# Kernel optimization log

Measured on AMD Instinct MI355X. Metric: run time of the kernel, lower is better.

Reference implementation:

```python
import jax, jax.numpy as jnp
import numpy as np

N_CHANNELS = 256
N_NEIGHBOURS = 262144
DIM = 3


def setup_inputs() -> dict:
    key = jax.random.key(0)
    k1, k2, k3 = jax.random.split(key, 3)
    h = jax.random.normal(k1, (N_CHANNELS, N_NEIGHBOURS), dtype=jnp.float32)
    rel_poss = jax.random.normal(k2, (DIM, N_NEIGHBOURS), dtype=jnp.float32)
    W = jax.random.normal(k3, (N_CHANNELS, N_CHANNELS), dtype=jnp.float32)
    return {"h": h, "rel_poss": rel_poss, "W": W}


def reference(h, rel_poss, W):
    # dists: [N], unit directions u: [dim, N]
    dists = jnp.linalg.norm(rel_poss, axis=0)
    u = rel_poss / dists
    # radial basis e_rbf(x, n, c=2) = (2/2)**0.5 * sin(n*x)/x = sin(n*x)/x, n = 1..K
    n = jnp.arange(1, N_CHANNELS + 1, dtype=h.dtype)
    radial_emb = jnp.sin(n[:, None] * dists[None, :]) / dists[None, :]  # [K, N]
    # channel-mixed features
    hp = W @ h  # [K, N]
    # per-neighbour: radial * feature scalar times rank-2 outer product u u^T, summed over neighbours
    m = radial_emb * hp  # [K, N]
    A = jnp.einsum('ki,di,ei->kde', m, u, u)  # [K, dim, dim]
    return A
```

## Files before the change

kernel.cpp:

```cpp
#include <hip/hip_runtime.h>
#include <hip/hip_bf16.h>

#define NCH      256
#define NNB      262144
#define BN       64
#define NTILES   (NNB / BN)
#define NB       512
#define ITPB     (NTILES / NB)
#define NENT     (NCH * 6)
#define NTHREADS 512

typedef __bf16        bf16x8 __attribute__((ext_vector_type(8)));
typedef float         f32x4  __attribute__((ext_vector_type(4)));
typedef unsigned int  u32x4  __attribute__((ext_vector_type(4)));
typedef unsigned int  u32x2  __attribute__((ext_vector_type(2)));
typedef short         v4s    __attribute__((ext_vector_type(4)));

union FragU  { u32x4 u; bf16x8 b; };
union Frag2U { u32x2 u; v4s    s; };

__device__ __forceinline__ unsigned pk2(float lo, float hi) {
    union { __hip_bfloat162 h2; unsigned u; } cv;
    cv.h2 = __float22bfloat162_rn(make_float2(lo, hi));
    return cv.u;
}

__device__ __forceinline__ const float* uni_ptr(const float* p) {
    unsigned long long u = (unsigned long long)p;
    unsigned lo = __builtin_amdgcn_readfirstlane((unsigned)u);
    unsigned hi = __builtin_amdgcn_readfirstlane((unsigned)(u >> 32));
    return (const float*)(((unsigned long long)hi << 32) | lo);
}

#define LBAR() do {                                                  \
    asm volatile("s_waitcnt lgkmcnt(0)" ::: "memory");               \
    __builtin_amdgcn_sched_barrier(0);                               \
    __builtin_amdgcn_s_barrier();                                    \
    __builtin_amdgcn_sched_barrier(0);                               \
} while (0)

#define CBODY(CB)                                                                  \
{                                                                                  \
    const int colb = (CB) * 16;                                                    \
    Frag2U gf;                                                                     \
    gf.u = *(const u32x2*)(gTP +                                                   \
           (((unsigned)(il * 128 + (colb + q * 4) * 2)) ^                          \
            (((unsigned)(il & 7)) << 3)));                                         \
    f32x4 hp0 = {0.f, 0.f, 0.f, 0.f}, hp1 = {0.f, 0.f, 0.f, 0.f};                  \
    const unsigned rb = (unsigned)((colb + il) * 512);                             \
    _Pragma("unroll")                                                              \
    for (int jb = 0; jb < 8; ++jb) {                                               \
        FragU f0;                                                                  \
        f0.u = *(const u32x4*)((const char*)htP +                                  \
               ((rb + (unsigned)(jb * 64 + q * 16)) ^ sw));                        \
        hp0 = __builtin_amdgcn_mfma_f32_16x16x32_bf16(f0.b, wf[0][jb].b, hp0, 0, 0, 0); \
        hp1 = __builtin_amdgcn_mfma_f32_16x16x32_bf16(f0.b, wf[1][jb].b, hp1, 0, 0, 0); \
    }                                                                              \
    f32x4 d4 = *(const f32x4*)(dtP + colb + q * 4);                                \
    f32x4 i4 = *(const f32x4*)(dtP + 64 + colb + q * 4);                           \
    Frag2U a0, a1;                                                                 \
    {                                                                              \
        float m0 = __sinf(fk0 * d4[0]) * i4[0] * hp0[0];                           \
        float m1 = __sinf(fk0 * d4[1]) * i4[1] * hp0[1];                           \
        float m2 = __sinf(fk0 * d4[2]) * i4[2] * hp0[2];                           \
        float m3 = __sinf(fk0 * d4[3]) * i4[3] * hp0[3];                           \
        a0.u[0] = pk2(m0, m1); a0.u[1] = pk2(m2, m3);                              \
        float n0 = __sinf(fk1 * d4[0]) * i4[0] * hp1[0];                           \
        float n1 = __sinf(fk1 * d4[1]) * i4[1] * hp1[1];                           \
        float n2 = __sinf(fk1 * d4[2]) * i4[2] * hp1[2];                           \
        float n3 = __sinf(fk1 * d4[3]) * i4[3] * hp1[3];                           \
        a1.u[0] = pk2(n0, n1); a1.u[1] = pk2(n2, n3);                              \
    }                                                                              \
    acc0 = __builtin_amdgcn_mfma_f32_16x16x16bf16_1k(a0.s, gf.s, acc0, 0, 0, 0);   \
    acc1 = __builtin_amdgcn_mfma_f32_16x16x16bf16_1k(a1.s, gf.s, acc1, 0, 0, 0);   \
}

#define CHUNK8_ISSUE(Q)                                                            \
    if (hasNext) {                                                                 \
        _Pragma("unroll")                                                          \
        for (int j = 0; j < 8; ++j)                                                \
            hc[j] = hwb[(size_t)((Q) * 8 + j) * NNB + baseN + c];                  \
    }

#define CHUNK8_PACK(Q)                                                             \
    if (hasNext) {                                                                 \
        u32x4 w0;                                                                  \
        w0[0] = pk2(hc[0], hc[1]); w0[1] = pk2(hc[2], hc[3]);                      \
        w0[2] = pk2(hc[4], hc[5]); w0[3] = pk2(hc[6], hc[7]);                      \
        *(u32x4*)((char*)htN +                                                     \
            (((unsigned)(c * 512 + wave * 64 + (Q) * 16)) ^ swc)) = w0;            \
    }

__global__ __launch_bounds__(NTHREADS, 2) void create_As_k1(
        const float* __restrict__ h, const float* __restrict__ rp,
        const float* __restrict__ W, float* __restrict__ ws)
{
    __shared__ unsigned short htile[2][BN * NCH];
    __shared__ unsigned short gT[2][16 * BN];
    __shared__ __align__(16) float dtab[2][2][BN];

    const int t    = threadIdx.x;
    const int wave = t >> 6;
    const int il   = t & 15;
    const int q    = (t >> 4) & 3;
    const int c    = t & 63;
    const int k0   = wave * 32;
    const unsigned sw  = ((unsigned)(il & 7)) << 4;
    const unsigned swc = ((unsigned)(c & 7)) << 4;
    const float fk0 = (float)(k0 + il + 1);
    const float fk1 = fk0 + 16.0f;

    #pragma unroll
    for (int z = 0; z < 2; ++z) ((unsigned*)gT)[t + z * NTHREADS] = 0u;

    FragU wf[2][8];
    #pragma unroll
    for (int kt = 0; kt < 2; ++kt) {
        const float* wr = W + (size_t)(k0 + kt * 16 + il) * NCH + q * 8;
        #pragma unroll
        for (int jb = 0; jb < 8; ++jb) {
            f32x4 a = *(const f32x4*)(wr + jb * 32);
            f32x4 b = *(const f32x4*)(wr + jb * 32 + 4);
            wf[kt][jb].u[0] = pk2(a[0], a[1]);
            wf[kt][jb].u[1] = pk2(a[2], a[3]);
            wf[kt][jb].u[2] = pk2(b[0], b[1]);
            wf[kt][jb].u[3] = pk2(b[2], b[3]);
        }
    }

    f32x4 acc0 = {0.f, 0.f, 0.f, 0.f};
    f32x4 acc1 = {0.f, 0.f, 0.f, 0.f};

    const float* hwb = uni_ptr(h + (size_t)(wave * 32) * NNB);

    const int d0 = blockIdx.x;

    __syncthreads();

    {
        const unsigned base = (unsigned)(d0 * BN);
        #pragma unroll
        for (int qq = 0; qq < 4; ++qq) {
            float hv[8];
            #pragma unroll
            for (int j = 0; j < 8; ++j)
                hv[j] = hwb[(size_t)(qq * 8 + j) * NNB + base + c];
            u32x4 w0;
            w0[0] = pk2(hv[0], hv[1]); w0[1] = pk2(hv[2], hv[3]);
            w0[2] = pk2(hv[4], hv[5]); w0[3] = pk2(hv[6], hv[7]);
            *(u32x4*)((char*)htile[0] +
                (((unsigned)(c * 512 + wave * 64 + qq * 16)) ^ swc)) = w0;
        }
        if (t < 64) {
            const unsigned ii = base + (unsigned)c;
            float gx = rp[ii], gy = rp[(size_t)NNB + ii], gz = rp[2 * (size_t)NNB + ii];
            float dd = sqrtf(gx * gx + gy * gy + gz * gz);
            float iv = 1.0f / dd;
            dtab[0][0][c] = dd; dtab[0][1][c] = iv;
            float i2 = iv * iv;
            float gg[6] = { gx * gx * i2, gx * gy * i2, gx * gz * i2,
                            gy * gy * i2, gy * gz * i2, gz * gz * i2 };
            #pragma unroll
            for (int de = 0; de < 6; ++de) {
                unsigned off = ((unsigned)(de * 128 + c * 2)) ^ (((unsigned)de) << 3);
                *(unsigned short*)((char*)gT[0] + off) =
                    (unsigned short)(pk2(gg[de], 0.f) & 0xffffu);
            }
        }
    }
    LBAR();

    #pragma unroll 1
    for (int it = 0; it < ITPB; ++it) {
        const int P = it & 1;
        const unsigned short* htP = htile[P];
        unsigned short*       htN = htile[P ^ 1];
        const char*  gTP = (const char*)gT[P];
        const float* dtP = &dtab[P][0][0];
        const bool hasNext = (it + 1 < ITPB);
        const unsigned baseN = (unsigned)((d0 + (it + 1) * NB) * BN);

        float gx = 0.f, gy = 0.f, gz = 0.f;
        if (hasNext && t < 64) {
            const unsigned ii = baseN + (unsigned)c;
            gx = rp[ii]; gy = rp[(size_t)NNB + ii]; gz = rp[2 * (size_t)NNB + ii];
        }

        float hc[8];
        CHUNK8_ISSUE(0)
        __builtin_amdgcn_sched_barrier(0);
        CBODY(0)
        __builtin_amdgcn_sched_barrier(0);
        CHUNK8_PACK(0) CHUNK8_ISSUE(1)
        __builtin_amdgcn_sched_barrier(0);
        CBODY(1)
        __builtin_amdgcn_sched_barrier(0);
        CHUNK8_PACK(1) CHUNK8_ISSUE(2)
        __builtin_amdgcn_sched_barrier(0);
        CBODY(2)
        __builtin_amdgcn_sched_barrier(0);
        CHUNK8_PACK(2) CHUNK8_ISSUE(3)
        __builtin_amdgcn_sched_barrier(0);
        CBODY(3)
        __builtin_amdgcn_sched_barrier(0);
        CHUNK8_PACK(3)
        if (hasNext && t < 64) {
            float dd = sqrtf(gx * gx + gy * gy + gz * gz);
            float iv = 1.0f / dd;
            dtab[P ^ 1][0][c] = dd; dtab[P ^ 1][1][c] = iv;
            float i2 = iv * iv;
            float gg[6] = { gx * gx * i2, gx * gy * i2, gx * gz * i2,
                            gy * gy * i2, gy * gz * i2, gz * gz * i2 };
            #pragma unroll
            for (int de = 0; de < 6; ++de) {
                unsigned off = ((unsigned)(de * 128 + c * 2)) ^ (((unsigned)de) << 3);
                *(unsigned short*)((char*)gT[P ^ 1] + off) =
                    (unsigned short)(pk2(gg[de], 0.f) & 0xffffu);
            }
        }
        LBAR();
    }

    if (il < 6) {
        float* dst = ws + (size_t)blockIdx.x * NENT;
        #pragma unroll
        for (int r = 0; r < 4; ++r) {
            dst[(k0 + q * 4 + r) * 6 + il]      = acc0[r];
            dst[(k0 + 16 + q * 4 + r) * 6 + il] = acc1[r];
        }
    }
}

__global__ void create_As_k2(const float* __restrict__ ws, float* __restrict__ out)
{
    __shared__ float red[8][64];
    const int eb = blockIdx.x;
    const int w  = threadIdx.x >> 6;
    const int l  = threadIdx.x & 63;
    float s = 0.f;
    #pragma unroll 4
    for (int b = w; b < NB; b += 8)
        s += ws[(size_t)b * NENT + (unsigned)(eb * 64 + l)];
    red[w][l] = s;
    __syncthreads();
    if (w == 0) {
        float v = red[0][l] + red[1][l] + red[2][l] + red[3][l]
                + red[4][l] + red[5][l] + red[6][l] + red[7][l];
        const int e  = eb * 64 + l;
        const int k  = e / 6;
        const int m6 = e - k * 6;
        const int d  = (m6 < 3) ? 0 : ((m6 < 5) ? 1 : 2);
        const int e2 = (m6 < 3) ? m6 : ((m6 < 5) ? (m6 - 2) : 2);
        out[k * 9 + d * 3 + e2] = v;
        if (d != e2) out[k * 9 + e2 * 3 + d] = v;
    }
}

extern "C" void kernel_launch(void* const* d_in, const int* in_sizes, int n_in,
                              void* d_out, int out_size, void* d_ws, size_t ws_size,
                              hipStream_t stream)
{
    const float* h  = (const float*)d_in[0];
    const float* rp = (const float*)d_in[1];
    const float* W  = (const float*)d_in[2];
    float* out = (float*)d_out;
    float* ws  = (float*)d_ws;

    hipLaunchKernelGGL(create_As_k1, dim3(NB), dim3(NTHREADS), 0, stream, h, rp, W, ws);
    hipLaunchKernelGGL(create_As_k2, dim3(NENT / 64), dim3(512), 0, stream, ws, out);
}
```

Before: 83.42 us.

## Double neighbour tile to 128 with float2 h loads and one block per CU

Raises the per-iteration neighbour tile from 64 to 128 columns and halves the grid to 256 blocks, each with occupancy hint 1. Global h loads become float2 per lane across two adjacent columns, and the LDS staging layout and swizzle are adjusted to match. The goal is fewer barriers per neighbour processed, wider global loads, and a longer software pipeline. In exchange, LDS use doubles and occupancy drops, which can expose latency. Note that the htile/gT/dtab declarations still use BN, so their sizes grow.

Measured after the change: 91.12 us. 9.2% more time.

```diff
diff --git a/kernel.cpp b/kernel.cpp
--- a/kernel.cpp
+++ b/kernel.cpp
@@ -3,15 +3,16 @@
 
 #define NCH      256
 #define NNB      262144
-#define BN       64
-#define NTILES   (NNB / BN)
-#define NB       512
-#define ITPB     (NTILES / NB)
+#define BN       128
+#define NDT      (NNB / BN)
+#define NB       256
+#define DTPB     (NDT / NB)
 #define NENT     (NCH * 6)
 #define NTHREADS 512
 
 typedef __bf16        bf16x8 __attribute__((ext_vector_type(8)));
 typedef float         f32x4  __attribute__((ext_vector_type(4)));
+typedef float         f32x2  __attribute__((ext_vector_type(2)));
 typedef unsigned int  u32x4  __attribute__((ext_vector_type(4)));
 typedef unsigned int  u32x2  __attribute__((ext_vector_type(2)));
 typedef short         v4s    __attribute__((ext_vector_type(4)));
@@ -44,7 +45,7 @@
     const int colb = (CB) * 16;                                                    \
     Frag2U gf;                                                                     \
     gf.u = *(const u32x2*)(gTP +                                                   \
-           (((unsigned)(il * 128 + (colb + q * 4) * 2)) ^                          \
+           (((unsigned)(il * 256 + (colb + q * 4) * 2)) ^                          \
             (((unsigned)(il & 7)) << 3)));                                         \
     f32x4 hp0 = {0.f, 0.f, 0.f, 0.f}, hp1 = {0.f, 0.f, 0.f, 0.f};                  \
     const unsigned rb = (unsigned)((colb + il) * 512);                             \
@@ -57,7 +58,7 @@
         hp1 = __builtin_amdgcn_mfma_f32_16x16x32_bf16(f0.b, wf[1][jb].b, hp1, 0, 0, 0); \
     }                                                                              \
     f32x4 d4 = *(const f32x4*)(dtP + colb + q * 4);                                \
-    f32x4 i4 = *(const f32x4*)(dtP + 64 + colb + q * 4);                           \
+    f32x4 i4 = *(const f32x4*)(dtP + BN + colb + q * 4);                           \
     Frag2U a0, a1;                                                                 \
     {                                                                              \
         float m0 = __sinf(fk0 * d4[0]) * i4[0] * hp0[0];                           \
@@ -75,23 +76,41 @@
     acc1 = __builtin_amdgcn_mfma_f32_16x16x16bf16_1k(a1.s, gf.s, acc1, 0, 0, 0);   \
 }
 
-#define CHUNK8_ISSUE(Q)                                                            \
+#define CHUNK4_ISSUE(Q)                                                            \
     if (hasNext) {                                                                 \
         _Pragma("unroll")                                                          \
-        for (int j = 0; j < 8; ++j)                                                \
-            hc[j] = hwb[(size_t)((Q) * 8 + j) * NNB + baseN + c];                  \
-    }
-
-#define CHUNK8_PACK(Q)                                                             \
+        for (int j2 = 0; j2 < 4; ++j2)                                             \
+            hc[j2] = *(const f32x2*)(hwb + (size_t)((Q) * 4 + j2) * NNB            \
+                                         + baseN + sc0);                           \
+    }
+
+#define CHUNK4_PACK(Q)                                                             \
     if (hasNext) {                                                                 \
-        u32x4 w0;                                                                  \
-        w0[0] = pk2(hc[0], hc[1]); w0[1] = pk2(hc[2], hc[3]);                      \
-        w0[2] = pk2(hc[4], hc[5]); w0[3] = pk2(hc[6], hc[7]);                      \
-        *(u32x4*)((char*)htN +                                                     \
-            (((unsigned)(c * 512 + wave * 64 + (Q) * 16)) ^ swc)) = w0;            \
-    }
-
-__global__ __launch_bounds__(NTHREADS, 2) void create_As_k1(
+        u32x2 wx, wy;                                                              \
+        wx[0] = pk2(hc[0][0], hc[1][0]); wx[1] = pk2(hc[2][0], hc[3][0]);          \
+        wy[0] = pk2(hc[0][1], hc[1][1]); wy[1] = pk2(hc[2][1], hc[3][1]);          \
+        const unsigned jo = (unsigned)(wave * 64 + (Q) * 8);                       \
+        *(u32x2*)((char*)htN + (((unsigned)(sc0 * 512)       + jo) ^ swp)) = wx;   \
+        *(u32x2*)((char*)htN + (((unsigned)(sc0 * 512 + 512) + jo) ^ swp)) = wy;   \
+    }
+
+#define GEOM(B)                                                                    \
+    if (t < 128) {                                                                 \
+        float dd = sqrtf(gx * gx + gy * gy + gz * gz);                             \
+        float iv = 1.0f / dd;                                                      \
+        dtab[B][0][t] = dd; dtab[B][1][t] = iv;                                    \
+        float i2 = iv * iv;                                                        \
+        float gg[6] = { gx * gx * i2, gx * gy * i2, gx * gz * i2,                  \
+                        gy * gy * i2, gy * gz * i2, gz * gz * i2 };                \
+        _Pragma("unroll")                                                          \
+        for (int de = 0; de < 6; ++de) {                                           \
+            unsigned off = ((unsigned)(de * 256 + t * 2)) ^ (((unsigned)de) << 3); \
+            *(unsigned short*)((char*)gT[B] + off) =                               \
+                (unsigned short)(pk2(gg[de], 0.f) & 0xffffu);                      \
+        }                                                                          \
+    }
+
+__global__ __launch_bounds__(NTHREADS, 1) void create_As_k1(
         const float* __restrict__ h, const float* __restrict__ rp,
         const float* __restrict__ W, float* __restrict__ ws)
 {
@@ -105,13 +124,14 @@
     const int q    = (t >> 4) & 3;
     const int c    = t & 63;
     const int k0   = wave * 32;
-    const unsigned sw  = ((unsigned)(il & 7)) << 4;
-    const unsigned swc = ((unsigned)(c & 7)) << 4;
+    const int sc0  = 2 * c;
+    const unsigned sw  = ((unsigned)((il >> 1) & 7)) << 4;
+    const unsigned swp = ((unsigned)(c & 7)) << 4;
     const float fk0 = (float)(k0 + il + 1);
     const float fk1 = fk0 + 16.0f;
 
     #pragma unroll
-    for (int z = 0; z < 2; ++z) ((unsigned*)gT)[t + z * NTHREADS] = 0u;
+    for (int z = 0; z < 4; ++z) ((unsigned*)gT)[t + z * NTHREADS] = 0u;
 
     FragU wf[2][8];
     #pragma unroll
@@ -140,84 +160,77 @@
     {
         const unsigned base = (unsigned)(d0 * BN);
         #pragma unroll
-        for (int qq = 0; qq < 4; ++qq) {
-            float hv[8];
+        for (int qq = 0; qq < 8; ++qq) {
+            f32x2 hv[4];
             #pragma unroll
-            for (int j = 0; j < 8; ++j)
-                hv[j] = hwb[(size_t)(qq * 8 + j) * NNB + base + c];
-            u32x4 w0;
-            w0[0] = pk2(hv[0], hv[1]); w0[1] = pk2(hv[2], hv[3]);
-            w0[2] = pk2(hv[4], hv[5]); w0[3] = pk2(hv[6], hv[7]);
-            *(u32x4*)((char*)htile[0] +
-                (((unsigned)(c * 512 + wave * 64 + qq * 16)) ^ swc)) = w0;
-        }
-        if (t < 64) {
-            const unsigned ii = base + (unsigned)c;
+            for (int j2 = 0; j2 < 4; ++j2)
+                hv[j2] = *(const f32x2*)(hwb + (size_t)(qq * 4 + j2) * NNB + base + sc0);
+            u32x2 wx, wy;
+            wx[0] = pk2(hv[0][0], hv[1][0]); wx[1] = pk2(hv[2][0], hv[3][0]);
+            wy[0] = pk2(hv[0][1], hv[1][1]); wy[1] = pk2(hv[2][1], hv[3][1]);
+            const unsigned jo = (unsigned)(wave * 64 + qq * 8);
+            *(u32x2*)((char*)htile[0] + (((unsigned)(sc0 * 512)       + jo) ^ swp)) = wx;
+            *(u32x2*)((char*)htile[0] + (((unsigned)(sc0 * 512 + 512) + jo) ^ swp)) = wy;
+        }
+        if (t < 128) {
+            const unsigned ii = base + (unsigned)t;
             float gx = rp[ii], gy = rp[(size_t)NNB + ii], gz = rp[2 * (size_t)NNB + ii];
-            float dd = sqrtf(gx * gx + gy * gy + gz * gz);
-            float iv = 1.0f / dd;
-            dtab[0][0][c] = dd; dtab[0][1][c] = iv;
-            float i2 = iv * iv;
-            float gg[6] = { gx * gx * i2, gx * gy * i2, gx * gz * i2,
-                            gy * gy * i2, gy * gz * i2, gz * gz * i2 };
-            #pragma unroll
-            for (int de = 0; de < 6; ++de) {
-                unsigned off = ((unsigned)(de * 128 + c * 2)) ^ (((unsigned)de) << 3);
-                *(unsigned short*)((char*)gT[0] + off) =
-                    (unsigned short)(pk2(gg[de], 0.f) & 0xffffu);
-            }
+            GEOM(0)
         }
     }
     LBAR();
 
     #pragma unroll 1
-    for (int it = 0; it < ITPB; ++it) {
+    for (int it = 0; it < DTPB; ++it) {
         const int P = it & 1;
         const unsigned short* htP = htile[P];
         unsigned short*       htN = htile[P ^ 1];
         const char*  gTP = (const char*)gT[P];
         const float* dtP = &dtab[P][0][0];
-        const bool hasNext = (it + 1 < ITPB);
+        const bool hasNext = (it + 1 < DTPB);
         const unsigned baseN = (unsigned)((d0 + (it + 1) * NB) * BN);
 
         float gx = 0.f, gy = 0.f, gz = 0.f;
-        if (hasNext && t < 64) {
-            const unsigned ii = baseN + (unsigned)c;
+        if (hasNext && t < 128) {
+            const unsigned ii = baseN + (unsigned)t;
             gx = rp[ii]; gy = rp[(size_t)NNB + ii]; gz = rp[2 * (size_t)NNB + ii];
         }
 
-        float hc[8];
-        CHUNK8_ISSUE(0)
+        f32x2 hc[4];
+        CHUNK4_ISSUE(0)
         __builtin_amdgcn_sched_barrier(0);
         CBODY(0)
         __builtin_amdgcn_sched_barrier(0);
-        CHUNK8_PACK(0) CHUNK8_ISSUE(1)
+        CHUNK4_PACK(0) CHUNK4_ISSUE(1)
         __builtin_amdgcn_sched_barrier(0);
         CBODY(1)
         __builtin_amdgcn_sched_barrier(0);
-        CHUNK8_PACK(1) CHUNK8_ISSUE(2)
+        CHUNK4_PACK(1) CHUNK4_ISSUE(2)
         __builtin_amdgcn_sched_barrier(0);
         CBODY(2)
         __builtin_amdgcn_sched_barrier(0);
-        CHUNK8_PACK(2) CHUNK8_ISSUE(3)
+        CHUNK4_PACK(2) CHUNK4_ISSUE(3)
         __builtin_amdgcn_sched_barrier(0);
         CBODY(3)
         __builtin_amdgcn_sched_barrier(0);
-        CHUNK8_PACK(3)
-        if (hasNext && t < 64) {
-            float dd = sqrtf(gx * gx + gy * gy + gz * gz);
-            float iv = 1.0f / dd;
-            dtab[P ^ 1][0][c] = dd; dtab[P ^ 1][1][c] = iv;
-            float i2 = iv * iv;
-            float gg[6] = { gx * gx * i2, gx * gy * i2, gx * gz * i2,
-                            gy * gy * i2, gy * gz * i2, gz * gz * i2 };
-            #pragma unroll
-            for (int de = 0; de < 6; ++de) {
-                unsigned off = ((unsigned)(de * 128 + c * 2)) ^ (((unsigned)de) << 3);
-                *(unsigned short*)((char*)gT[P ^ 1] + off) =
-                    (unsigned short)(pk2(gg[de], 0.f) & 0xffffu);
-            }
-        }
+        CHUNK4_PACK(3) CHUNK4_ISSUE(4)
+        __builtin_amdgcn_sched_barrier(0);
+        CBODY(4)
+        __builtin_amdgcn_sched_barrier(0);
+        CHUNK4_PACK(4) CHUNK4_ISSUE(5)
+        __builtin_amdgcn_sched_barrier(0);
+        CBODY(5)
+        __builtin_amdgcn_sched_barrier(0);
+        CHUNK4_PACK(5) CHUNK4_ISSUE(6)
+        __builtin_amdgcn_sched_barrier(0);
+        CBODY(6)
+        __builtin_amdgcn_sched_barrier(0);
+        CHUNK4_PACK(6) CHUNK4_ISSUE(7)
+        __builtin_amdgcn_sched_barrier(0);
+        CBODY(7)
+        __builtin_amdgcn_sched_barrier(0);
+        CHUNK4_PACK(7)
+        if (hasNext) { GEOM(P ^ 1) }
         LBAR();
     }
 
```

## Halve block to 4 waves, each computing 64 output channels

Applied to the files above, without the earlier changes.

Block size drops from 512 to 256 threads, and each wave now owns 64 channels of W instead of 32. Each LDS A-fragment of h is therefore reused across four MFMA weight tiles rather than two. The h prefetch for the next tile is restructured into two 16-element register buffers that are issued two chunks ahead. This cuts LDS reads per MFMA and wave count, at the cost of doubling the W fragment registers and prefetch registers, which may lower occupancy or cause spills.

New measurement: 283.7 us. 240% more time.

```diff
diff --git a/kernel.cpp b/kernel.cpp
--- a/kernel.cpp
+++ b/kernel.cpp
@@ -8,7 +8,7 @@
 #define NB       512
 #define ITPB     (NTILES / NB)
 #define NENT     (NCH * 6)
-#define NTHREADS 512
+#define NTHREADS 256
 
 typedef __bf16        bf16x8 __attribute__((ext_vector_type(8)));
 typedef float         f32x4  __attribute__((ext_vector_type(4)));
@@ -46,7 +46,8 @@
     gf.u = *(const u32x2*)(gTP +                                                   \
            (((unsigned)(il * 128 + (colb + q * 4) * 2)) ^                          \
             (((unsigned)(il & 7)) << 3)));                                         \
-    f32x4 hp0 = {0.f, 0.f, 0.f, 0.f}, hp1 = {0.f, 0.f, 0.f, 0.f};                  \
+    f32x4 hp0 = {0.f,0.f,0.f,0.f}, hp1 = {0.f,0.f,0.f,0.f};                        \
+    f32x4 hp2 = {0.f,0.f,0.f,0.f}, hp3 = {0.f,0.f,0.f,0.f};                        \
     const unsigned rb = (unsigned)((colb + il) * 512);                             \
     _Pragma("unroll")                                                              \
     for (int jb = 0; jb < 8; ++jb) {                                               \
@@ -55,40 +56,57 @@
                ((rb + (unsigned)(jb * 64 + q * 16)) ^ sw));                        \
         hp0 = __builtin_amdgcn_mfma_f32_16x16x32_bf16(f0.b, wf[0][jb].b, hp0, 0, 0, 0); \
         hp1 = __builtin_amdgcn_mfma_f32_16x16x32_bf16(f0.b, wf[1][jb].b, hp1, 0, 0, 0); \
+        hp2 = __builtin_amdgcn_mfma_f32_16x16x32_bf16(f0.b, wf[2][jb].b, hp2, 0, 0, 0); \
+        hp3 = __builtin_amdgcn_mfma_f32_16x16x32_bf16(f0.b, wf[3][jb].b, hp3, 0, 0, 0); \
     }                                                                              \
     f32x4 d4 = *(const f32x4*)(dtP + colb + q * 4);                                \
     f32x4 i4 = *(const f32x4*)(dtP + 64 + colb + q * 4);                           \
-    Frag2U a0, a1;                                                                 \
     {                                                                              \
-        float m0 = __sinf(fk0 * d4[0]) * i4[0] * hp0[0];                           \
-        float m1 = __sinf(fk0 * d4[1]) * i4[1] * hp0[1];                           \
-        float m2 = __sinf(fk0 * d4[2]) * i4[2] * hp0[2];                           \
-        float m3 = __sinf(fk0 * d4[3]) * i4[3] * hp0[3];                           \
-        a0.u[0] = pk2(m0, m1); a0.u[1] = pk2(m2, m3);                              \
-        float n0 = __sinf(fk1 * d4[0]) * i4[0] * hp1[0];                           \
-        float n1 = __sinf(fk1 * d4[1]) * i4[1] * hp1[1];                           \
-        float n2 = __sinf(fk1 * d4[2]) * i4[2] * hp1[2];                           \
-        float n3 = __sinf(fk1 * d4[3]) * i4[3] * hp1[3];                           \
-        a1.u[0] = pk2(n0, n1); a1.u[1] = pk2(n2, n3);                              \
+        Frag2U a;                                                                  \
+        float m0 = __sinf(fkb * d4[0]) * i4[0] * hp0[0];                           \
+        float m1 = __sinf(fkb * d4[1]) * i4[1] * hp0[1];                           \
+        float m2 = __sinf(fkb * d4[2]) * i4[2] * hp0[2];                           \
+        float m3 = __sinf(fkb * d4[3]) * i4[3] * hp0[3];                           \
+        a.u[0] = pk2(m0, m1); a.u[1] = pk2(m2, m3);                                \
+        acc0 = __builtin_amdgcn_mfma_f32_16x16x16bf16_1k(a.s, gf.s, acc0, 0, 0, 0);\
+        m0 = __sinf((fkb + 16.f) * d4[0]) * i4[0] * hp1[0];                        \
+        m1 = __sinf((fkb + 16.f) * d4[1]) * i4[1] * hp1[1];                        \
+        m2 = __sinf((fkb + 16.f) * d4[2]) * i4[2] * hp1[2];                        \
+        m3 = __sinf((fkb + 16.f) * d4[3]) * i4[3] * hp1[3];                        \
+        a.u[0] = pk2(m0, m1); a.u[1] = pk2(m2, m3);                                \
+        acc1 = __builtin_amdgcn_mfma_f32_16x16x16bf16_1k(a.s, gf.s, acc1, 0, 0, 0);\
+        m0 = __sinf((fkb + 32.f) * d4[0]) * i4[0] * hp2[0];                        \
+        m1 = __sinf((fkb + 32.f) * d4[1]) * i4[1] * hp2[1];                        \
+        m2 = __sinf((fkb + 32.f) * d4[2]) * i4[2] * hp2[2];                        \
+        m3 = __sinf((fkb + 32.f) * d4[3]) * i4[3] * hp2[3];                        \
+        a.u[0] = pk2(m0, m1); a.u[1] = pk2(m2, m3);                                \
+        acc2 = __builtin_amdgcn_mfma_f32_16x16x16bf16_1k(a.s, gf.s, acc2, 0, 0, 0);\
+        m0 = __sinf((fkb + 48.f) * d4[0]) * i4[0] * hp3[0];                        \
+        m1 = __sinf((fkb + 48.f) * d4[1]) * i4[1] * hp3[1];                        \
+        m2 = __sinf((fkb + 48.f) * d4[2]) * i4[2] * hp3[2];                        \
+        m3 = __sinf((fkb + 48.f) * d4[3]) * i4[3] * hp3[3];                        \
+        a.u[0] = pk2(m0, m1); a.u[1] = pk2(m2, m3);                                \
+        acc3 = __builtin_amdgcn_mfma_f32_16x16x16bf16_1k(a.s, gf.s, acc3, 0, 0, 0);\
     }                                                                              \
-    acc0 = __builtin_amdgcn_mfma_f32_16x16x16bf16_1k(a0.s, gf.s, acc0, 0, 0, 0);   \
-    acc1 = __builtin_amdgcn_mfma_f32_16x16x16bf16_1k(a1.s, gf.s, acc1, 0, 0, 0);   \
-}
-
-#define CHUNK8_ISSUE(Q)                                                            \
+}
+
+#define CHUNK16_ISSUE(DST, Q)                                                      \
     if (hasNext) {                                                                 \
         _Pragma("unroll")                                                          \
-        for (int j = 0; j < 8; ++j)                                                \
-            hc[j] = hwb[(size_t)((Q) * 8 + j) * NNB + baseN + c];                  \
-    }
-
-#define CHUNK8_PACK(Q)                                                             \
+        for (int j = 0; j < 16; ++j)                                               \
+            DST[j] = hwb[(size_t)((Q) * 16 + j) * NNB + baseN + c];                \
+    }
+
+#define CHUNK16_PACK(SRC, Q)                                                       \
     if (hasNext) {                                                                 \
-        u32x4 w0;                                                                  \
-        w0[0] = pk2(hc[0], hc[1]); w0[1] = pk2(hc[2], hc[3]);                      \
-        w0[2] = pk2(hc[4], hc[5]); w0[3] = pk2(hc[6], hc[7]);                      \
-        *(u32x4*)((char*)htN +                                                     \
-            (((unsigned)(c * 512 + wave * 64 + (Q) * 16)) ^ swc)) = w0;            \
+        u32x4 w0, w1;                                                              \
+        w0[0] = pk2(SRC[0],  SRC[1]);  w0[1] = pk2(SRC[2],  SRC[3]);               \
+        w0[2] = pk2(SRC[4],  SRC[5]);  w0[3] = pk2(SRC[6],  SRC[7]);               \
+        w1[0] = pk2(SRC[8],  SRC[9]);  w1[1] = pk2(SRC[10], SRC[11]);              \
+        w1[2] = pk2(SRC[12], SRC[13]); w1[3] = pk2(SRC[14], SRC[15]);              \
+        const unsigned boff = (unsigned)(c * 512 + wave * 128 + (Q) * 32);         \
+        *(u32x4*)((char*)htN + ((boff)      ^ swc)) = w0;                          \
+        *(u32x4*)((char*)htN + ((boff + 16) ^ swc)) = w1;                          \
     }
 
 __global__ __launch_bounds__(NTHREADS, 2) void create_As_k1(
@@ -104,18 +122,17 @@
     const int il   = t & 15;
     const int q    = (t >> 4) & 3;
     const int c    = t & 63;
-    const int k0   = wave * 32;
+    const int k0   = wave * 64;
     const unsigned sw  = ((unsigned)(il & 7)) << 4;
     const unsigned swc = ((unsigned)(c & 7)) << 4;
-    const float fk0 = (float)(k0 + il + 1);
-    const float fk1 = fk0 + 16.0f;
+    const float fkb = (float)(k0 + il + 1);
 
     #pragma unroll
-    for (int z = 0; z < 2; ++z) ((unsigned*)gT)[t + z * NTHREADS] = 0u;
-
-    FragU wf[2][8];
+    for (int z = 0; z < 4; ++z) ((unsigned*)gT)[t + z * NTHREADS] = 0u;
+
+    FragU wf[4][8];
     #pragma unroll
-    for (int kt = 0; kt < 2; ++kt) {
+    for (int kt = 0; kt < 4; ++kt) {
         const float* wr = W + (size_t)(k0 + kt * 16 + il) * NCH + q * 8;
         #pragma unroll
         for (int jb = 0; jb < 8; ++jb) {
@@ -128,10 +145,12 @@
         }
     }
 
-    f32x4 acc0 = {0.f, 0.f, 0.f, 0.f};
-    f32x4 acc1 = {0.f, 0.f, 0.f, 0.f};
-
-    const float* hwb = uni_ptr(h + (size_t)(wave * 32) * NNB);
+    f32x4 acc0 = {0.f,0.f,0.f,0.f};
+    f32x4 acc1 = {0.f,0.f,0.f,0.f};
+    f32x4 acc2 = {0.f,0.f,0.f,0.f};
+    f32x4 acc3 = {0.f,0.f,0.f,0.f};
+
+    const float* hwb = uni_ptr(h + (size_t)(wave * 64) * NNB);
 
     const int d0 = blockIdx.x;
 
@@ -141,15 +160,18 @@
         const unsigned base = (unsigned)(d0 * BN);
         #pragma unroll
         for (int qq = 0; qq < 4; ++qq) {
-            float hv[8];
+            float hv[16];
             #pragma unroll
-            for (int j = 0; j < 8; ++j)
-                hv[j] = hwb[(size_t)(qq * 8 + j) * NNB + base + c];
-            u32x4 w0;
-            w0[0] = pk2(hv[0], hv[1]); w0[1] = pk2(hv[2], hv[3]);
-            w0[2] = pk2(hv[4], hv[5]); w0[3] = pk2(hv[6], hv[7]);
-            *(u32x4*)((char*)htile[0] +
-                (((unsigned)(c * 512 + wave * 64 + qq * 16)) ^ swc)) = w0;
+            for (int j = 0; j < 16; ++j)
+                hv[j] = hwb[(size_t)(qq * 16 + j) * NNB + base + c];
+            u32x4 w0, w1;
+            w0[0] = pk2(hv[0],  hv[1]);  w0[1] = pk2(hv[2],  hv[3]);
+            w0[2] = pk2(hv[4],  hv[5]);  w0[3] = pk2(hv[6],  hv[7]);
+            w1[0] = pk2(hv[8],  hv[9]);  w1[1] = pk2(hv[10], hv[11]);
+            w1[2] = pk2(hv[12], hv[13]); w1[3] = pk2(hv[14], hv[15]);
+            const unsigned boff = (unsigned)(c * 512 + wave * 128 + qq * 32);
+            *(u32x4*)((char*)htile[0] + ((boff)      ^ swc)) = w0;
+            *(u32x4*)((char*)htile[0] + ((boff + 16) ^ swc)) = w1;
         }
         if (t < 64) {
             const unsigned ii = base + (unsigned)c;
@@ -186,24 +208,25 @@
             gx = rp[ii]; gy = rp[(size_t)NNB + ii]; gz = rp[2 * (size_t)NNB + ii];
         }
 
-        float hc[8];
-        CHUNK8_ISSUE(0)
+        float hA[16], hB[16];
+        CHUNK16_ISSUE(hA, 0)
+        CHUNK16_ISSUE(hB, 1)
         __builtin_amdgcn_sched_barrier(0);
         CBODY(0)
         __builtin_amdgcn_sched_barrier(0);
-        CHUNK8_PACK(0) CHUNK8_ISSUE(1)
+        CHUNK16_PACK(hA, 0) CHUNK16_ISSUE(hA, 2)
         __builtin_amdgcn_sched_barrier(0);
         CBODY(1)
         __builtin_amdgcn_sched_barrier(0);
-        CHUNK8_PACK(1) CHUNK8_ISSUE(2)
+        CHUNK16_PACK(hB, 1) CHUNK16_ISSUE(hB, 3)
         __builtin_amdgcn_sched_barrier(0);
         CBODY(2)
         __builtin_amdgcn_sched_barrier(0);
-        CHUNK8_PACK(2) CHUNK8_ISSUE(3)
+        CHUNK16_PACK(hA, 2)
         __builtin_amdgcn_sched_barrier(0);
         CBODY(3)
         __builtin_amdgcn_sched_barrier(0);
-        CHUNK8_PACK(3)
+        CHUNK16_PACK(hB, 3)
         if (hasNext && t < 64) {
             float dd = sqrtf(gx * gx + gy * gy + gz * gz);
             float iv = 1.0f / dd;
@@ -225,8 +248,10 @@
         float* dst = ws + (size_t)blockIdx.x * NENT;
         #pragma unroll
         for (int r = 0; r < 4; ++r) {
-            dst[(k0 + q * 4 + r) * 6 + il]      = acc0[r];
+            dst[(k0 +      q * 4 + r) * 6 + il] = acc0[r];
             dst[(k0 + 16 + q * 4 + r) * 6 + il] = acc1[r];
+            dst[(k0 + 32 + q * 4 + r) * 6 + il] = acc2[r];
+            dst[(k0 + 48 + q * 4 + r) * 6 + il] = acc3[r];
         }
     }
 }
```
